# Kernel tuning notes

Hardware: AMD Instinct MI355X
Metric: run time of the kernel (lower is better)

Reference implementation:

```python
import jax, jax.numpy as jnp
import numpy as np

BS, N, HD, NW = 4, 512, 64, 2
IN_DIM = 2 * HD * NW  # 256, fc1 input
EMB = HD              # node embedding dim (fc2 output)

# static off-diagonal indices (mask = ~eye)
_rows, _cols = np.nonzero(~np.eye(N, dtype=bool))
ROWS = jnp.asarray(_rows)
COLS = jnp.asarray(_cols)


def _leaky(x):
    return jnp.where(x > 0, x, 0.01 * x)


def setup_inputs() -> dict:
    key = jax.random.key(0)
    ks = jax.random.split(key, 10)
    s = lambda fan_in: 1.0 / np.sqrt(fan_in)
    return {
        "node_features": jax.random.normal(ks[0], (BS, N, IN_DIM), jnp.float32),
        "fc1_w": jax.random.normal(ks[1], (IN_DIM, 2 * HD), jnp.float32) * s(IN_DIM),
        "fc1_b": jnp.zeros((2 * HD,), jnp.float32),
        "fc2_w": jax.random.normal(ks[2], (2 * HD, EMB), jnp.float32) * s(2 * HD),
        "fc2_b": jnp.zeros((EMB,), jnp.float32),
        "e1_w": jax.random.normal(ks[3], (2 * EMB, EMB), jnp.float32) * s(2 * EMB),
        "e1_b": jnp.zeros((EMB,), jnp.float32),
        "e2_w": jax.random.normal(ks[4], (EMB, 2), jnp.float32) * s(EMB),
        "e2_b": jnp.zeros((2,), jnp.float32),
    }


def reference(node_features, fc1_w, fc1_b, fc2_w, fc2_b, e1_w, e1_b, e2_w, e2_b):
    # fc head (dropout = identity at inference)
    h = _leaky(jnp.einsum('bnf,fh->bnh', node_features, fc1_w) + fc1_b)
    emb = _leaky(jnp.einsum('bnh,hd->bnd', h, fc2_w) + fc2_b)  # [bs, N, EMB]

    # O(N^2) pairwise broadcast: hi - hj and hi * hj, concat -> edge MLP
    hi = emb[:, :, None, :]                 # [bs, N, 1, EMB]
    hj = emb[:, None, :, :]                 # [bs, 1, N, EMB]
    edge_in = jnp.concatenate([hi - hj, hi * hj], axis=-1)  # [bs, N, N, 2*EMB]

    eh = jnp.maximum(jnp.einsum('bijf,fh->bijh', edge_in, e1_w) + e1_b, 0.0)
    logits = jnp.einsum('bijh,hk->bijk', eh, e2_w) + e2_b    # [bs, N, N, 2]
    edge_prob = jax.nn.softmax(logits, axis=-1)

    adjacency_matrix = edge_prob[..., 1]                     # [bs, N, N]
    # masked gather of off-diagonal entries, both class probs, flattened per batch
    prediction = edge_prob[:, ROWS, COLS, :].reshape(edge_prob.shape[0], -1)
    return adjacency_matrix, prediction, emb
```

## Files before the change

### kernel.cpp

```cpp
#include <hip/hip_runtime.h>
#include <hip/hip_bf16.h>

#define BSZ 4
#define NN 512
#define INDIM 256
#define H1 128
#define EMBD 64

#define PRED_OFF  (BSZ*NN*NN)
#define PRED_PER_B (NN*(NN-1)*2)
#define EMB_OFF   (PRED_OFF + BSZ*PRED_PER_B)

typedef __attribute__((ext_vector_type(8))) short bf16x8;
typedef __attribute__((ext_vector_type(4))) float f32x4;

static __device__ __forceinline__ short bfs(float x) {
  return (short)__builtin_bit_cast(unsigned short, __float2bfloat16(x));
}
static __device__ __forceinline__ bf16x8 pack8(float4 a, float4 b) {
  bf16x8 r;
  r[0] = bfs(a.x); r[1] = bfs(a.y); r[2] = bfs(a.z); r[3] = bfs(a.w);
  r[4] = bfs(b.x); r[5] = bfs(b.y); r[6] = bfs(b.z); r[7] = bfs(b.w);
  return r;
}

template<bool WS>
__global__ __launch_bounds__(256) void k1_embed(
    const float* __restrict__ nf, const float* __restrict__ fc1w,
    const float* __restrict__ fc1b, const float* __restrict__ fc2w,
    const float* __restrict__ fc2b, float* __restrict__ out,
    unsigned short* __restrict__ ebf)
{
  __shared__ float nfs[4][INDIM];
  __shared__ float hs[4][H1];
  const int t = threadIdx.x;
  const int nb = blockIdx.x * 4;

  {
    const int nd = t >> 6, off = (t & 63) * 4;
    *reinterpret_cast<float4*>(&nfs[nd][off]) =
        *reinterpret_cast<const float4*>(nf + (size_t)(nb + nd) * INDIM + off);
  }
  __syncthreads();
  {
    const int c = t & 127, grp = t >> 7;
    float a0 = 0.f, a1 = 0.f;
    for (int f = 0; f < INDIM; ++f) {
      const float w = fc1w[f * H1 + c];
      a0 = fmaf(nfs[grp][f], w, a0);
      a1 = fmaf(nfs[grp + 2][f], w, a1);
    }
    const float bb = fc1b[c];
    a0 += bb; a1 += bb;
    hs[grp][c]     = a0 > 0.f ? a0 : 0.01f * a0;
    hs[grp + 2][c] = a1 > 0.f ? a1 : 0.01f * a1;
  }
  __syncthreads();
  {
    const int d = t & 63, nd = t >> 6;
    float acc = 0.f;
    for (int f = 0; f < H1; ++f) acc = fmaf(hs[nd][f], fc2w[f * EMBD + d], acc);
    acc += fc2b[d];
    const float e = acc > 0.f ? acc : 0.01f * acc;
    const size_t idx = (size_t)(nb + nd) * EMBD + d;
    out[EMB_OFF + idx] = e;
    if (WS) ebf[idx] = (unsigned short)bfs(e);
  }
}

template<bool WS>
__global__ __launch_bounds__(64, 4) void k2_edges(
    const float* __restrict__ e1w, const float* __restrict__ e1b,
    const float* __restrict__ e2w, const float* __restrict__ e2b,
    float* __restrict__ out, const unsigned short* __restrict__ ebf)
{
  __shared__ float embi[64];
  __shared__ float ash[64];
  __shared__ float wds[64];
  __shared__ __align__(16) float part[256][4];
  const int t = threadIdx.x;
  const int blk = blockIdx.x;
  const int b = blk >> 10;
  const int rr = blk & 1023;
  const int i = rr >> 1;
  const int jh = rr & 1;
  const float* __restrict__ Ef = out + EMB_OFF;

  embi[t] = Ef[((size_t)(b * NN) + i) * EMBD + t];
  wds[t]  = e2w[2 * t + 1] - e2w[2 * t];
  __syncthreads();

  {
    float acc = 0.f;
#pragma unroll 8
    for (int dd = 0; dd < EMBD; ++dd)
      acc = fmaf(embi[dd], e1w[dd * 64 + t], acc);
    ash[t] = acc + e1b[t];
  }
  __syncthreads();

  const int lg = t >> 4, ll = t & 15;

  f32x4 ci[4], wd4[4];
#pragma unroll
  for (int mt = 0; mt < 4; ++mt) {
    ci[mt]  = *reinterpret_cast<const f32x4*>(&ash[mt * 16 + lg * 4]);
    wd4[mt] = *reinterpret_cast<const f32x4*>(&wds[mt * 16 + lg * 4]);
  }

  bf16x8 afr[4][2];
#pragma unroll
  for (int ks = 0; ks < 2; ++ks) {
    float e8[8];
    *reinterpret_cast<float4*>(&e8[0]) =
        *reinterpret_cast<const float4*>(&embi[ks * 32 + lg * 8]);
    *reinterpret_cast<float4*>(&e8[4]) =
        *reinterpret_cast<const float4*>(&embi[ks * 32 + lg * 8 + 4]);
#pragma unroll
    for (int mt = 0; mt < 4; ++mt) {
      const int h = mt * 16 + ll;
      bf16x8 a;
#pragma unroll
      for (int q = 0; q < 8; ++q) {
        const int d = ks * 32 + lg * 8 + q;
        a[q] = bfs(fmaf(e8[q], e1w[(64 + d) * 64 + h], -e1w[d * 64 + h]));
      }
      afr[mt][ks] = a;
    }
  }

  auto loadB = [&](int j0, bf16x8& o0, bf16x8& o1) {
    if (WS) {
      const unsigned short* p =
          ebf + ((size_t)(b * NN) + j0 + ll) * EMBD + lg * 8;
      o0 = *reinterpret_cast<const bf16x8*>(p);
      o1 = *reinterpret_cast<const bf16x8*>(p + 32);
    } else {
      const float* ef = Ef + ((size_t)(b * NN) + j0 + ll) * EMBD + lg * 8;
      const float4 fa = *reinterpret_cast<const float4*>(ef);
      const float4 fb = *reinterpret_cast<const float4*>(ef + 4);
      const float4 fc = *reinterpret_cast<const float4*>(ef + 32);
      const float4 fd = *reinterpret_cast<const float4*>(ef + 36);
      o0 = pack8(fa, fb);
      o1 = pack8(fc, fd);
    }
  };

  auto process = [&](const bf16x8& b0, const bf16x8& b1, int nt) {
    f32x4 acc[4];
#pragma unroll
    for (int mt = 0; mt < 4; ++mt)
      acc[mt] = __builtin_amdgcn_mfma_f32_16x16x32_bf16(afr[mt][0], b0, ci[mt], 0, 0, 0);
#pragma unroll
    for (int mt = 0; mt < 4; ++mt)
      acc[mt] = __builtin_amdgcn_mfma_f32_16x16x32_bf16(afr[mt][1], b1, acc[mt], 0, 0, 0);

    float lp0 = 0.f, lp1 = 0.f, lp2 = 0.f, lp3 = 0.f;
#pragma unroll
    for (int mt = 0; mt < 4; ++mt) {
      lp0 = fmaf(fmaxf(acc[mt][0], 0.f), wd4[mt][0], lp0);
      lp1 = fmaf(fmaxf(acc[mt][1], 0.f), wd4[mt][1], lp1);
      lp2 = fmaf(fmaxf(acc[mt][2], 0.f), wd4[mt][2], lp2);
      lp3 = fmaf(fmaxf(acc[mt][3], 0.f), wd4[mt][3], lp3);
    }
    part[nt * 16 + ll][lg] = (lp0 + lp1) + (lp2 + lp3);
  };

  const int jbase = jh * 256;
  bf16x8 a0, a1, c0, c1;
  loadB(jbase, a0, a1);
  loadB(jbase + 16, c0, c1);

  for (int base = 0; base < 16; base += 2) {
    process(a0, a1, base);
    if (base + 2 < 16) loadB(jbase + (base + 2) * 16, a0, a1);
    process(c0, c1, base + 1);
    if (base + 3 < 16) loadB(jbase + (base + 3) * 16, c0, c1);
  }
  __syncthreads();

  const float ldbias = e2b[1] - e2b[0];
  const size_t adj_base = ((size_t)(b * NN) + i) * NN + jbase;
  const size_t pred_base =
      (size_t)PRED_OFF + (size_t)b * PRED_PER_B + (size_t)i * (NN - 1) * 2;

#pragma unroll
  for (int e4 = 0; e4 < 4; ++e4) {
    const int jl = e4 * 64 + t;
    const f32x4 p4 = *reinterpret_cast<const f32x4*>(&part[jl][0]);
    const float x = (p4[0] + p4[1]) + (p4[2] + p4[3]) + ldbias;
    const float e = __builtin_amdgcn_exp2f(x * -1.44269504f);
    const float p1 = __builtin_amdgcn_rcpf(1.f + e);
    const float p0 = e * p1;

    const int j = jbase + jl;
    out[adj_base + jl] = p1;
    if (j != i) {
      const int jj = j - (j > i ? 1 : 0);
      *reinterpret_cast<float2*>(out + pred_base + (size_t)jj * 2) =
          make_float2(p0, p1);
    }
  }
}

extern "C" void kernel_launch(void* const* d_in, const int* in_sizes, int n_in,
                              void* d_out, int out_size, void* d_ws, size_t ws_size,
                              hipStream_t stream) {
  const float* nf   = (const float*)d_in[0];
  const float* fc1w = (const float*)d_in[1];
  const float* fc1b = (const float*)d_in[2];
  const float* fc2w = (const float*)d_in[3];
  const float* fc2b = (const float*)d_in[4];
  const float* e1w  = (const float*)d_in[5];
  const float* e1b  = (const float*)d_in[6];
  const float* e2w  = (const float*)d_in[7];
  const float* e2b  = (const float*)d_in[8];
  float* out = (float*)d_out;
  unsigned short* ebf = (unsigned short*)d_ws;
  const bool use_ws = ws_size >= (size_t)BSZ * NN * EMBD * sizeof(unsigned short);

  if (use_ws) {
    k1_embed<true><<<BSZ * NN / 4, 256, 0, stream>>>(nf, fc1w, fc1b, fc2w, fc2b, out, ebf);
    k2_edges<true><<<BSZ * NN * 2, 64, 0, stream>>>(e1w, e1b, e2w, e2b, out, ebf);
  } else {
    k1_embed<false><<<BSZ * NN / 4, 256, 0, stream>>>(nf, fc1w, fc1b, fc2w, fc2b, out, nullptr);
    k2_edges<false><<<BSZ * NN * 2, 64, 0, stream>>>(e1w, e1b, e2w, e2b, out, nullptr);
  }
}
```

Measured before the change: 109.9 us.

## Precompute per-row edge MLP A-fragments and bias in a separate prep kernel

Adds a prep kernel that, once per node, computes the bf16 MFMA A-fragments (emb_i*W2 - W1) and the per-row bias term (emb_i*W1 + b1) and stores them in workspace in fragment order. The edge kernel then loads these directly instead of recomputing them in both half-row blocks, which removes the duplicated scattered weight loads and FMA setup. The cost is an extra kernel launch, about 16 MB of extra workspace traffic, and a larger workspace requirement; if the workspace is too small, the old path is used.

```diff
diff --git a/kernel.cpp b/kernel.cpp
--- a/kernel.cpp
+++ b/kernel.cpp
@@ -10,6 +10,10 @@
 #define PRED_OFF  (BSZ*NN*NN)
 #define PRED_PER_B (NN*(NN-1)*2)
 #define EMB_OFF   (PRED_OFF + BSZ*PRED_PER_B)
+
+#define WS_BPR_OFF  (1u << 20)
+#define WS_AWS_OFF  (20u << 20)
+#define WS_NEEDED   ((size_t)(21u << 20))
 
 typedef __attribute__((ext_vector_type(8))) short bf16x8;
 typedef __attribute__((ext_vector_type(4))) float f32x4;
@@ -68,15 +72,49 @@
   }
 }
 
+__global__ __launch_bounds__(64) void k1b_prep(
+    const float* __restrict__ Ef, const float* __restrict__ e1w,
+    const float* __restrict__ e1b, unsigned short* __restrict__ bpr,
+    float* __restrict__ aws)
+{
+  __shared__ float embi[64];
+  const int t = threadIdx.x;
+  const int blk = blockIdx.x;
+  embi[t] = Ef[(size_t)blk * EMBD + t];
+  __syncthreads();
+
+  const int mt = t >> 4, ll = t & 15;
+  unsigned short* __restrict__ bo = bpr + (size_t)blk * 4096;
+
+  float a = 0.f;
+#pragma unroll
+  for (int ks = 0; ks < 2; ++ks)
+#pragma unroll
+    for (int lg = 0; lg < 4; ++lg) {
+      bf16x8 v;
+#pragma unroll
+      for (int q = 0; q < 8; ++q) {
+        const int d = ks * 32 + lg * 8 + q;
+        const float w1v = e1w[d * 64 + t];
+        const float w2v = e1w[(64 + d) * 64 + t];
+        a = fmaf(embi[d], w1v, a);
+        v[q] = bfs(fmaf(embi[d], w2v, -w1v));
+      }
+      *reinterpret_cast<bf16x8*>(bo + ((mt * 2 + ks) * 4 + lg) * 128 + ll * 8) = v;
+    }
+  aws[(size_t)blk * EMBD + t] = a + e1b[t];
+}
+
 template<bool WS>
 __global__ __launch_bounds__(64, 4) void k2_edges(
     const float* __restrict__ e1w, const float* __restrict__ e1b,
     const float* __restrict__ e2w, const float* __restrict__ e2b,
-    float* __restrict__ out, const unsigned short* __restrict__ ebf)
+    float* __restrict__ out, const unsigned short* __restrict__ ebf,
+    const unsigned short* __restrict__ bpr, const float* __restrict__ aws)
 {
   __shared__ float embi[64];
+  __shared__ float wds[64];
   __shared__ float ash[64];
-  __shared__ float wds[64];
   __shared__ __align__(16) float part[256][4];
   const int t = threadIdx.x;
   const int blk = blockIdx.x;
@@ -86,46 +124,59 @@
   const int jh = rr & 1;
   const float* __restrict__ Ef = out + EMB_OFF;
 
-  embi[t] = Ef[((size_t)(b * NN) + i) * EMBD + t];
-  wds[t]  = e2w[2 * t + 1] - e2w[2 * t];
-  __syncthreads();
-
-  {
-    float acc = 0.f;
+  wds[t] = e2w[2 * t + 1] - e2w[2 * t];
+  if (!WS) embi[t] = Ef[((size_t)(b * NN) + i) * EMBD + t];
+  __syncthreads();
+
+  const int lg = t >> 4, ll = t & 15;
+
+  f32x4 ci[4], wd4[4];
+  bf16x8 afr[4][2];
+
+  if (WS) {
+    const unsigned short* __restrict__ bo = bpr + (size_t)(b * NN + i) * 4096;
+    const float* __restrict__ ao = aws + (size_t)(b * NN + i) * EMBD;
+#pragma unroll
+    for (int mt = 0; mt < 4; ++mt) {
+#pragma unroll
+      for (int ks = 0; ks < 2; ++ks)
+        afr[mt][ks] = *reinterpret_cast<const bf16x8*>(
+            bo + ((mt * 2 + ks) * 4 + lg) * 128 + ll * 8);
+      ci[mt]  = *reinterpret_cast<const f32x4*>(ao + mt * 16 + lg * 4);
+      wd4[mt] = *reinterpret_cast<const f32x4*>(&wds[mt * 16 + lg * 4]);
+    }
+  } else {
+    {
+      float acc = 0.f;
 #pragma unroll 8
-    for (int dd = 0; dd < EMBD; ++dd)
-      acc = fmaf(embi[dd], e1w[dd * 64 + t], acc);
-    ash[t] = acc + e1b[t];
-  }
-  __syncthreads();
-
-  const int lg = t >> 4, ll = t & 15;
-
-  f32x4 ci[4], wd4[4];
-#pragma unroll
-  for (int mt = 0; mt < 4; ++mt) {
-    ci[mt]  = *reinterpret_cast<const f32x4*>(&ash[mt * 16 + lg * 4]);
-    wd4[mt] = *reinterpret_cast<const f32x4*>(&wds[mt * 16 + lg * 4]);
-  }
-
-  bf16x8 afr[4][2];
-#pragma unroll
-  for (int ks = 0; ks < 2; ++ks) {
-    float e8[8];
-    *reinterpret_cast<float4*>(&e8[0]) =
-        *reinterpret_cast<const float4*>(&embi[ks * 32 + lg * 8]);
-    *reinterpret_cast<float4*>(&e8[4]) =
-        *reinterpret_cast<const float4*>(&embi[ks * 32 + lg * 8 + 4]);
+      for (int dd = 0; dd < EMBD; ++dd)
+        acc = fmaf(embi[dd], e1w[dd * 64 + t], acc);
+      ash[t] = acc + e1b[t];
+    }
+    __syncthreads();
 #pragma unroll
     for (int mt = 0; mt < 4; ++mt) {
-      const int h = mt * 16 + ll;
-      bf16x8 a;
-#pragma unroll
-      for (int q = 0; q < 8; ++q) {
-        const int d = ks * 32 + lg * 8 + q;
-        a[q] = bfs(fmaf(e8[q], e1w[(64 + d) * 64 + h], -e1w[d * 64 + h]));
+      ci[mt]  = *reinterpret_cast<const f32x4*>(&ash[mt * 16 + lg * 4]);
+      wd4[mt] = *reinterpret_cast<const f32x4*>(&wds[mt * 16 + lg * 4]);
+    }
+#pragma unroll
+    for (int ks = 0; ks < 2; ++ks) {
+      float e8[8];
+      *reinterpret_cast<float4*>(&e8[0]) =
+          *reinterpret_cast<const float4*>(&embi[ks * 32 + lg * 8]);
+      *reinterpret_cast<float4*>(&e8[4]) =
+          *reinterpret_cast<const float4*>(&embi[ks * 32 + lg * 8 + 4]);
+#pragma unroll
+      for (int mt = 0; mt < 4; ++mt) {
+        const int h = mt * 16 + ll;
+        bf16x8 a;
+#pragma unroll
+        for (int q = 0; q < 8; ++q) {
+          const int d = ks * 32 + lg * 8 + q;
+          a[q] = bfs(fmaf(e8[q], e1w[(64 + d) * 64 + h], -e1w[d * 64 + h]));
+        }
+        afr[mt][ks] = a;
       }
-      afr[mt][ks] = a;
     }
   }
 
@@ -216,14 +267,18 @@
   const float* e2w  = (const float*)d_in[7];
   const float* e2b  = (const float*)d_in[8];
   float* out = (float*)d_out;
-  unsigned short* ebf = (unsigned short*)d_ws;
-  const bool use_ws = ws_size >= (size_t)BSZ * NN * EMBD * sizeof(unsigned short);
+  char* wsb = (char*)d_ws;
+  unsigned short* ebf = (unsigned short*)wsb;
+  unsigned short* bpr = (unsigned short*)(wsb + WS_BPR_OFF);
+  float* aws = (float*)(wsb + WS_AWS_OFF);
+  const bool use_ws = ws_size >= WS_NEEDED;
 
   if (use_ws) {
     k1_embed<true><<<BSZ * NN / 4, 256, 0, stream>>>(nf, fc1w, fc1b, fc2w, fc2b, out, ebf);
-    k2_edges<true><<<BSZ * NN * 2, 64, 0, stream>>>(e1w, e1b, e2w, e2b, out, ebf);
+    k1b_prep<<<BSZ * NN, 64, 0, stream>>>(out + EMB_OFF, e1w, e1b, bpr, aws);
+    k2_edges<true><<<BSZ * NN * 2, 64, 0, stream>>>(e1w, e1b, e2w, e2b, out, ebf, bpr, aws);
   } else {
     k1_embed<false><<<BSZ * NN / 4, 256, 0, stream>>>(nf, fc1w, fc1b, fc2w, fc2b, out, nullptr);
-    k2_edges<false><<<BSZ * NN * 2, 64, 0, stream>>>(e1w, e1b, e2w, e2b, out, nullptr);
-  }
-}
+    k2_edges<false><<<BSZ * NN * 2, 64, 0, stream>>>(e1w, e1b, e2w, e2b, out, nullptr, nullptr, nullptr);
+  }
+}
```

Result: slower. 118.7 us (+8.0%).
